# Kernel tuning notes

Measured on AMD Instinct MI355X. Metric: run time of the kernel, lower is better.

Reference implementation:

```python
import jax, jax.numpy as jnp
import numpy as np

SIZE = 100
NUM_PARAMS = 5
DEPTH = 10            # complete binary tree: 2**DEPTH - 1 = 1023 nodes, 512 leaves
NUM_TREES = 1024
NUM_NODES = 2 ** DEPTH - 1


def setup_inputs() -> dict:
    key = jax.random.key(0)
    ks = jax.random.split(key, 7)
    times = jax.random.uniform(ks[0], (NUM_TREES, NUM_NODES), dtype=jnp.float32) + 0.1
    # Linear(1, size): weight column vector + bias
    Qw = jax.random.normal(ks[1], (SIZE,), dtype=jnp.float32) * 0.5
    Qb = jax.random.normal(ks[2], (SIZE,), dtype=jnp.float32) * 0.1
    # Linear(size, size): scaled so deep relu chain stays stable
    Ww = jax.random.normal(ks[3], (SIZE, SIZE), dtype=jnp.float32) * (0.5 / np.sqrt(SIZE))
    Wb = jax.random.normal(ks[4], (SIZE,), dtype=jnp.float32) * 0.1
    # Linear(size, num_params)
    Pw = jax.random.normal(ks[5], (NUM_PARAMS, SIZE), dtype=jnp.float32) * (1.0 / np.sqrt(SIZE))
    Pb = jax.random.normal(ks[6], (NUM_PARAMS,), dtype=jnp.float32) * 0.1
    return {"times": times, "Qw": Qw, "Qb": Qb, "Ww": Ww, "Wb": Wb, "Pw": Pw, "Pb": Pb}


def reference(times, Qw, Qb, Ww, Wb, Pw, Pb):
    """Batched, level-synchronous version of gRNN.traverse over complete binary trees.

    times: [B, 2**D - 1] node times in heap order (node i -> children 2i+1, 2i+2).
    Leaf:     h = relu(Q(t))
    Internal: h = relu(W(h_left + h_right) + Q(t))
    Root output projected to num_params. Same math as the recursive torch code.
    """
    B, N = times.shape
    D = int(np.log2(N + 1))
    # leaf level (deepest): Q(t) = t * Qw + Qb  (Linear(1, size))
    s = 2 ** (D - 1) - 1
    h = jax.nn.relu(times[:, s:s + 2 ** (D - 1), None] * Qw + Qb)  # [B, 2^(D-1), size]
    for d in range(D - 2, -1, -1):  # fixed small loop over tree depth
        s = 2 ** d - 1
        t = times[:, s:s + 2 ** d, None]                 # [B, 2^d, 1]
        comb = h[:, 0::2] + h[:, 1::2]                   # left + right children
        h = jax.nn.relu(jnp.einsum('bns,os->bno', comb, Ww) + Wb + t * Qw + Qb)
    root = h[:, 0]                                       # [B, size]
    return root @ Pw.T + Pb                              # [B, num_params]
```

## Files before the change

kernel.cpp:

```cpp
#include <hip/hip_runtime.h>

typedef _Float16 h8 __attribute__((ext_vector_type(8)));
typedef _Float16 h4 __attribute__((ext_vector_type(4)));
typedef float f4 __attribute__((ext_vector_type(4)));
typedef unsigned int uint32;

#define NT 7
#define KC 4
#define HSTRIDE 108

__global__ __launch_bounds__(256, 2)
void grnn_fused(const float* __restrict__ times,
                const float* __restrict__ Qw,
                const float* __restrict__ Qb,
                const float* __restrict__ Ww,
                const float* __restrict__ Wb,
                const float* __restrict__ Pw,
                const float* __restrict__ Pb,
                float* __restrict__ out)
{
  __shared__ __align__(16) _Float16 Hs[256][HSTRIDE];
  __shared__ __align__(8)  _Float16 ts[1026];
  __shared__ __align__(16) float qw_s[128];
  __shared__ __align__(16) float qb_s[128];

  const int tid  = threadIdx.x;
  const int wave = tid >> 6;
  const int lane = tid & 63;
  const int l15  = lane & 15;
  const int kg   = lane >> 4;
  const int tree = blockIdx.x;

  {
    const float* tg = times + tree * 1023;
    for (int i = tid; i < 1023; i += 256) ts[1 + i] = (_Float16)tg[i];
    if (tid == 0) ts[0] = (_Float16)0.f;
    if (tid < 128) {
      float qw = 0.f, qb = 0.f;
      if (tid < 100) { qw = Qw[tid]; qb = Qb[tid]; }
      qw_s[tid] = qw; qb_s[tid] = qb;
    }
  }

  h8 wf[NT][KC];
  #pragma unroll
  for (int nt = 0; nt < NT; ++nt) {
    const int r = nt * 16 + l15;
    #pragma unroll
    for (int kc = 0; kc < KC; ++kc) {
      h8 v;
      #pragma unroll
      for (int j = 0; j < 8; ++j) v[j] = (_Float16)0.f;
      if (r < 100) {
        const int kb = kc * 32 + kg * 8;
        if (kc < 3) {
          const f4 w0 = *(const f4*)&Ww[r * 100 + kb];
          const f4 w1 = *(const f4*)&Ww[r * 100 + kb + 4];
          #pragma unroll
          for (int j = 0; j < 4; ++j) {
            v[j]     = (_Float16)w0[j];
            v[j + 4] = (_Float16)w1[j];
          }
        } else if (kg == 0) {
          const f4 w0 = *(const f4*)&Ww[r * 100 + 96];
          #pragma unroll
          for (int j = 0; j < 4; ++j) v[j] = (_Float16)w0[j];
          v[4] = (_Float16)Qw[r];
          v[5] = (_Float16)(Qb[r] + Wb[r]);
        }
      }
      wf[nt][kc] = v;
    }
  }
  __syncthreads();

#define DO_MT(MT) do {                                                        \
    _Pragma("unroll")                                                         \
    for (int nt_ = 0; nt_ < NT; ++nt_) {                                      \
      f4 acc_ = {0.f, 0.f, 0.f, 0.f};                                         \
      _Pragma("unroll")                                                       \
      for (int kc_ = 0; kc_ < KC; ++kc_)                                      \
        acc_ = __builtin_amdgcn_mfma_f32_16x16x32_f16(wf[nt_][kc_], af[kc_],  \
                                                      acc_, 0, 0, 0);         \
      if (nt_ < 6 || kg == 0) {                                               \
        h4 hv_ = {(_Float16)fmaxf(acc_[0], 0.f),                              \
                  (_Float16)fmaxf(acc_[1], 0.f),                              \
                  (_Float16)fmaxf(acc_[2], 0.f),                              \
                  (_Float16)fmaxf(acc_[3], 0.f)};                             \
        *(h4*)&Hs[(MT) * 16 + l15][nt_ * 16 + kg * 4] = hv_;                  \
      }                                                                       \
    }                                                                         \
  } while (0)

#define LOAD_AFR(MT, S) do {                                                  \
    const int m2_ = ((MT) * 16 + l15) * 2;                                    \
    _Pragma("unroll")                                                         \
    for (int kc_ = 0; kc_ < 3; ++kc_) {                                       \
      const int kb_ = kc_ * 32 + kg * 8;                                      \
      h4 a0_ = *(const h4*)&Hs[m2_][kb_];                                     \
      h4 b0_ = *(const h4*)&Hs[m2_][kb_ + 4];                                 \
      h4 a1_ = *(const h4*)&Hs[m2_ + 1][kb_];                                 \
      h4 b1_ = *(const h4*)&Hs[m2_ + 1][kb_ + 4];                             \
      h4 lo_ = a0_ + a1_, hi_ = b0_ + b1_;                                    \
      af[kc_] = __builtin_shufflevector(lo_, hi_, 0, 1, 2, 3, 4, 5, 6, 7);    \
    }                                                                         \
    if (kg == 0) {                                                            \
      h4 a0_ = *(const h4*)&Hs[m2_][96];                                      \
      h4 a1_ = *(const h4*)&Hs[m2_ + 1][96];                                  \
      h4 lo_ = a0_ + a1_;                                                     \
      h4 hi_ = {ts[1 + (S) + (MT) * 16 + l15], (_Float16)1.f,                 \
                (_Float16)0.f, (_Float16)0.f};                                \
      af[3] = __builtin_shufflevector(lo_, hi_, 0, 1, 2, 3, 4, 5, 6, 7);      \
    } else {                                                                  \
      _Pragma("unroll")                                                       \
      for (int j_ = 0; j_ < 8; ++j_) af[3][j_] = (_Float16)0.f;               \
    }                                                                         \
  } while (0)

  #pragma unroll 1
  for (int i = 0; i < 4; ++i) {
    const int mt = wave + 4 * i;
    const int m  = mt * 16 + l15;
    const uint32 tp = *(const uint32*)&ts[512 + 2 * m];
    const float t0 = (float)*(const _Float16*)&tp;
    const float t1 = (float)*((const _Float16*)&tp + 1);
    h8 af[KC];
    #pragma unroll
    for (int kc = 0; kc < KC; ++kc) {
      const int kb = kc * 32 + kg * 8;
      const f4 qwa = *(const f4*)&qw_s[kb];
      const f4 qwb = *(const f4*)&qw_s[kb + 4];
      const f4 qba = *(const f4*)&qb_s[kb];
      const f4 qbb = *(const f4*)&qb_s[kb + 4];
      #pragma unroll
      for (int j = 0; j < 4; ++j) {
        float h0 = fmaxf(t0 * qwa[j] + qba[j], 0.f);
        float h1 = fmaxf(t1 * qwa[j] + qba[j], 0.f);
        af[kc][j] = (_Float16)(h0 + h1);
        float g0 = fmaxf(t0 * qwb[j] + qbb[j], 0.f);
        float g1 = fmaxf(t1 * qwb[j] + qbb[j], 0.f);
        af[kc][j + 4] = (_Float16)(g0 + g1);
      }
    }
    if (kg == 0) {
      af[3][4] = ts[1 + 255 + m];
      af[3][5] = (_Float16)1.f;
      af[3][6] = (_Float16)0.f;
      af[3][7] = (_Float16)0.f;
    }
    DO_MT(mt);
  }

  #pragma unroll 1
  for (int d = 7; d >= 0; --d) {
    const int s  = (1 << d) - 1;
    const int nm = (d >= 4) ? (1 << (d - 4)) : 1;
    const bool mine = wave < (nm < 4 ? nm : 4);
    h8 af[KC];
    if (mine) LOAD_AFR(wave, s);
    __syncthreads();
    if (mine) {
      DO_MT(wave);
      if (nm == 8) {
        LOAD_AFR(wave + 4, s);
        DO_MT(wave + 4);
      }
    }
    __syncthreads();
  }

  if (tid < 160) {
    const int p = tid >> 5;
    const int j = tid & 31;
    float sum = 0.f;
    #pragma unroll
    for (int c = 0; c < 4; ++c) {
      const int o = j + 32 * c;
      if (o < 100) sum += (float)Hs[0][o] * Pw[p * 100 + o];
    }
    sum += __shfl_down(sum, 16, 32);
    sum += __shfl_down(sum, 8, 32);
    sum += __shfl_down(sum, 4, 32);
    sum += __shfl_down(sum, 2, 32);
    sum += __shfl_down(sum, 1, 32);
    if (j == 0) out[tree * 5 + p] = sum + Pb[p];
  }
#undef DO_MT
#undef LOAD_AFR
}

extern "C" void kernel_launch(void* const* d_in, const int* in_sizes, int n_in,
                              void* d_out, int out_size, void* d_ws, size_t ws_size,
                              hipStream_t stream) {
  (void)n_in; (void)out_size; (void)d_ws; (void)ws_size;
  const float* times = (const float*)d_in[0];
  const float* Qw = (const float*)d_in[1];
  const float* Qb = (const float*)d_in[2];
  const float* Ww = (const float*)d_in[3];
  const float* Wb = (const float*)d_in[4];
  const float* Pw = (const float*)d_in[5];
  const float* Pb = (const float*)d_in[6];
  float* outp = (float*)d_out;
  const int B = in_sizes[0] / 1023;
  grnn_fused<<<dim3(B), dim3(256), 0, stream>>>(times, Qw, Qb, Ww, Wb, Pw, Pb, outp);
}
```

Measured before the change: 101.5 us.

## Process each tree with a single wavefront and pre-sum sibling pairs via shuffles

Each block now handles one tree with a single 64-lane wavefront instead of four waves. All per-level `__syncthreads` barriers go away, and the wave walks every tile of each tree level in sequence. Before writing, sibling node outputs are added together with a lane xor-shuffle, so shared memory holds half as many rows, and the next level loads pre-combined rows directly instead of adding pairs. The root projection becomes a single-wave reduction. The cost is far fewer resident waves per tree and per SIMD, so MFMA latency has less overlap from other waves.

Result: slower. 112.5 us (+10.9%).

```diff
diff --git a/kernel.cpp b/kernel.cpp
--- a/kernel.cpp
+++ b/kernel.cpp
@@ -7,9 +7,9 @@
 
 #define NT 7
 #define KC 4
-#define HSTRIDE 108
-
-__global__ __launch_bounds__(256, 2)
+#define HSTRIDE 104
+
+__global__ __launch_bounds__(64, 1)
 void grnn_fused(const float* __restrict__ times,
                 const float* __restrict__ Qw,
                 const float* __restrict__ Qb,
@@ -19,26 +19,30 @@
                 const float* __restrict__ Pb,
                 float* __restrict__ out)
 {
-  __shared__ __align__(16) _Float16 Hs[256][HSTRIDE];
+  __shared__ __align__(16) _Float16 Cs[128][HSTRIDE];
   __shared__ __align__(8)  _Float16 ts[1026];
   __shared__ __align__(16) float qw_s[128];
   __shared__ __align__(16) float qb_s[128];
 
-  const int tid  = threadIdx.x;
-  const int wave = tid >> 6;
-  const int lane = tid & 63;
+  const int lane = threadIdx.x;
   const int l15  = lane & 15;
   const int kg   = lane >> 4;
   const int tree = blockIdx.x;
 
   {
     const float* tg = times + tree * 1023;
-    for (int i = tid; i < 1023; i += 256) ts[1 + i] = (_Float16)tg[i];
-    if (tid == 0) ts[0] = (_Float16)0.f;
-    if (tid < 128) {
+    #pragma unroll
+    for (int i = 0; i < 16; ++i) {
+      const int idx = lane + 64 * i;
+      if (idx < 1023) ts[1 + idx] = (_Float16)tg[idx];
+    }
+    if (lane == 0) ts[0] = (_Float16)0.f;
+    #pragma unroll
+    for (int i = 0; i < 2; ++i) {
+      const int idx = lane + 64 * i;
       float qw = 0.f, qb = 0.f;
-      if (tid < 100) { qw = Qw[tid]; qb = Qb[tid]; }
-      qw_s[tid] = qw; qb_s[tid] = qb;
+      if (idx < 100) { qw = Qw[idx]; qb = Qb[idx]; }
+      qw_s[idx] = qw; qb_s[idx] = qb;
     }
   }
 
@@ -72,7 +76,6 @@
       wf[nt][kc] = v;
     }
   }
-  __syncthreads();
 
 #define DO_MT(MT) do {                                                        \
     _Pragma("unroll")                                                         \
@@ -80,34 +83,48 @@
       f4 acc_ = {0.f, 0.f, 0.f, 0.f};                                         \
       _Pragma("unroll")                                                       \
       for (int kc_ = 0; kc_ < KC; ++kc_)                                      \
-        acc_ = __builtin_amdgcn_mfma_f32_16x16x32_f16(wf[nt_][kc_], af[kc_],  \
-                                                      acc_, 0, 0, 0);         \
+        acc_ = __builtin_amdgcn_mfma_f32_16x16x32_f16(wf[nt_][kc_],           \
+                                                      af[kc_], acc_, 0,0,0);  \
       if (nt_ < 6 || kg == 0) {                                               \
         h4 hv_ = {(_Float16)fmaxf(acc_[0], 0.f),                              \
                   (_Float16)fmaxf(acc_[1], 0.f),                              \
                   (_Float16)fmaxf(acc_[2], 0.f),                              \
                   (_Float16)fmaxf(acc_[3], 0.f)};                             \
-        *(h4*)&Hs[(MT) * 16 + l15][nt_ * 16 + kg * 4] = hv_;                  \
+        uint2 u_ = __builtin_bit_cast(uint2, hv_);                            \
+        u_.x = __shfl_xor(u_.x, 1, 64);                                       \
+        u_.y = __shfl_xor(u_.y, 1, 64);                                       \
+        hv_ = hv_ + __builtin_bit_cast(h4, u_);                               \
+        if ((l15 & 1) == 0)                                                   \
+          *(h4*)&Cs[(MT) * 8 + (l15 >> 1)][nt_ * 16 + kg * 4] = hv_;          \
       }                                                                       \
     }                                                                         \
   } while (0)
 
+#define DO_MT_ROOT() do {                                                     \
+    _Pragma("unroll")                                                         \
+    for (int nt_ = 0; nt_ < NT; ++nt_) {                                      \
+      f4 acc_ = {0.f, 0.f, 0.f, 0.f};                                         \
+      _Pragma("unroll")                                                       \
+      for (int kc_ = 0; kc_ < KC; ++kc_)                                      \
+        acc_ = __builtin_amdgcn_mfma_f32_16x16x32_f16(wf[nt_][kc_],           \
+                                                      af[kc_], acc_, 0,0,0);  \
+      if ((nt_ < 6 || kg == 0) && l15 == 0) {                                 \
+        h4 hv_ = {(_Float16)fmaxf(acc_[0], 0.f),                              \
+                  (_Float16)fmaxf(acc_[1], 0.f),                              \
+                  (_Float16)fmaxf(acc_[2], 0.f),                              \
+                  (_Float16)fmaxf(acc_[3], 0.f)};                             \
+        *(h4*)&Cs[0][nt_ * 16 + kg * 4] = hv_;                                \
+      }                                                                       \
+    }                                                                         \
+  } while (0)
+
 #define LOAD_AFR(MT, S) do {                                                  \
-    const int m2_ = ((MT) * 16 + l15) * 2;                                    \
+    const int row_ = (MT) * 16 + l15;                                         \
     _Pragma("unroll")                                                         \
-    for (int kc_ = 0; kc_ < 3; ++kc_) {                                       \
-      const int kb_ = kc_ * 32 + kg * 8;                                      \
-      h4 a0_ = *(const h4*)&Hs[m2_][kb_];                                     \
-      h4 b0_ = *(const h4*)&Hs[m2_][kb_ + 4];                                 \
-      h4 a1_ = *(const h4*)&Hs[m2_ + 1][kb_];                                 \
-      h4 b1_ = *(const h4*)&Hs[m2_ + 1][kb_ + 4];                             \
-      h4 lo_ = a0_ + a1_, hi_ = b0_ + b1_;                                    \
-      af[kc_] = __builtin_shufflevector(lo_, hi_, 0, 1, 2, 3, 4, 5, 6, 7);    \
-    }                                                                         \
+    for (int kc_ = 0; kc_ < 3; ++kc_)                                         \
+      af[kc_] = *(const h8*)&Cs[row_][kc_ * 32 + kg * 8];                     \
     if (kg == 0) {                                                            \
-      h4 a0_ = *(const h4*)&Hs[m2_][96];                                      \
-      h4 a1_ = *(const h4*)&Hs[m2_ + 1][96];                                  \
-      h4 lo_ = a0_ + a1_;                                                     \
+      h4 lo_ = *(const h4*)&Cs[row_][96];                                     \
       h4 hi_ = {ts[1 + (S) + (MT) * 16 + l15], (_Float16)1.f,                 \
                 (_Float16)0.f, (_Float16)0.f};                                \
       af[3] = __builtin_shufflevector(lo_, hi_, 0, 1, 2, 3, 4, 5, 6, 7);      \
@@ -118,9 +135,8 @@
   } while (0)
 
   #pragma unroll 1
-  for (int i = 0; i < 4; ++i) {
-    const int mt = wave + 4 * i;
-    const int m  = mt * 16 + l15;
+  for (int i = 0; i < 16; ++i) {
+    const int m = i * 16 + l15;
     const uint32 tp = *(const uint32*)&ts[512 + 2 * m];
     const float t0 = (float)*(const _Float16*)&tp;
     const float t1 = (float)*((const _Float16*)&tp + 1);
@@ -148,44 +164,41 @@
       af[3][6] = (_Float16)0.f;
       af[3][7] = (_Float16)0.f;
     }
-    DO_MT(mt);
+    DO_MT(i);
   }
 
   #pragma unroll 1
-  for (int d = 7; d >= 0; --d) {
+  for (int d = 7; d >= 1; --d) {
     const int s  = (1 << d) - 1;
     const int nm = (d >= 4) ? (1 << (d - 4)) : 1;
-    const bool mine = wave < (nm < 4 ? nm : 4);
+    #pragma unroll 1
+    for (int i = 0; i < nm; ++i) {
+      h8 af[KC];
+      LOAD_AFR(i, s);
+      DO_MT(i);
+    }
+  }
+
+  {
     h8 af[KC];
-    if (mine) LOAD_AFR(wave, s);
-    __syncthreads();
-    if (mine) {
-      DO_MT(wave);
-      if (nm == 8) {
-        LOAD_AFR(wave + 4, s);
-        DO_MT(wave + 4);
-      }
-    }
-    __syncthreads();
-  }
-
-  if (tid < 160) {
-    const int p = tid >> 5;
-    const int j = tid & 31;
-    float sum = 0.f;
-    #pragma unroll
-    for (int c = 0; c < 4; ++c) {
-      const int o = j + 32 * c;
-      if (o < 100) sum += (float)Hs[0][o] * Pw[p * 100 + o];
-    }
-    sum += __shfl_down(sum, 16, 32);
-    sum += __shfl_down(sum, 8, 32);
-    sum += __shfl_down(sum, 4, 32);
-    sum += __shfl_down(sum, 2, 32);
-    sum += __shfl_down(sum, 1, 32);
-    if (j == 0) out[tree * 5 + p] = sum + Pb[p];
+    LOAD_AFR(0, 0);
+    DO_MT_ROOT();
+  }
+
+  #pragma unroll 1
+  for (int p = 0; p < 5; ++p) {
+    float v = (float)Cs[0][lane] * Pw[p * 100 + lane];
+    if (lane < 36) v += (float)Cs[0][64 + lane] * Pw[p * 100 + 64 + lane];
+    v += __shfl_xor(v, 32, 64);
+    v += __shfl_xor(v, 16, 64);
+    v += __shfl_xor(v, 8, 64);
+    v += __shfl_xor(v, 4, 64);
+    v += __shfl_xor(v, 2, 64);
+    v += __shfl_xor(v, 1, 64);
+    if (lane == 0) out[tree * 5 + p] = v + Pb[p];
   }
 #undef DO_MT
+#undef DO_MT_ROOT
 #undef LOAD_AFR
 }
 
@@ -202,5 +215,5 @@
   const float* Pb = (const float*)d_in[6];
   float* outp = (float*)d_out;
   const int B = in_sizes[0] / 1023;
-  grnn_fused<<<dim3(B), dim3(256), 0, stream>>>(times, Qw, Qb, Ww, Wb, Pw, Pb, outp);
+  grnn_fused<<<dim3(B), dim3(64), 0, stream>>>(times, Qw, Qb, Ww, Wb, Pw, Pb, outp);
 }
```
